# Optimization experiments

Measured on AMD Instinct MI355X. Metric: run time of the kernel, lower is better.

## Reference

```python
import jax, jax.numpy as jnp
import numpy as np

B, T, E, H, D = 1, 2048, 1024, 16, 64  # H*D == E required by module


def setup_inputs() -> dict:
    key = jax.random.key(0)
    ks = jax.random.split(key, 9)
    s_in = (2.0 / E) ** 0.5
    return {
        "x": jax.random.normal(ks[0], (B, T, E), jnp.float32),
        "wq": jax.random.normal(ks[1], (H * D, E), jnp.float32) * E ** -0.5,
        "wk": jax.random.normal(ks[2], (H * D, E), jnp.float32) * E ** -0.5,
        "wv": jax.random.normal(ks[3], (H * D, E), jnp.float32) * E ** -0.5,
        "wr": jax.random.normal(ks[4], (H, E, T), jnp.float32) * s_in,
        "wvr": jax.random.normal(ks[5], (H * D, E), jnp.float32) * E ** -0.5,
        "wj": jax.random.normal(ks[6], (E, E), jnp.float32) * E ** -0.5,
        "gate": jnp.zeros((H, 3), jnp.float32),
        "wo": jax.random.normal(ks[7], (E, H * D), jnp.float32) * E ** -0.5,
    }


def reference(x, wq, wk, wv, wr, wvr, wj, gate, wo):
    Bx, Tx, Ex = x.shape
    Hh = wr.shape[0]
    Dd = wq.shape[0] // Hh
    scale = 1.0 / Dd ** 0.5
    neg = -jnp.inf
    mask = jnp.triu(jnp.ones((Tx, Tx), bool), 1)  # True above diagonal

    def heads(w):  # (B,T,H*D) -> (B,H,T,D)
        return (x @ w.T).reshape(Bx, Tx, Hh, Dd).transpose(0, 2, 1, 3)

    # --- branch 1: standard causal QKV attention ---
    q, k, v = heads(wq), heads(wk), heads(wv)
    qkv_attn = jnp.einsum('bhqd,bhkd->bhqk', q, k) * scale
    qkv_attn = jnp.where(mask, neg, qkv_attn)
    qkv_out = jnp.einsum('bhqk,bhkd->bhqd', jax.nn.softmax(qkv_attn, axis=-1), v)

    # --- branch 2: RRPRAM learned per-position scores ---
    rv = heads(wvr)
    r = jnp.einsum('bte,het->bht', x, wr[:, :, :Tx])  # (B,H,T) key scores
    r_attn = jnp.where(mask, neg, (r * scale)[:, :, None, :])  # (B,H,T,T)
    rrp_out = jnp.einsum('bhqk,bhkd->bhqd', jax.nn.softmax(r_attn, axis=-1), rv)

    # --- branch 3: Janus self-resonance ---
    echo = x @ wj.T            # (B,T,E)
    echo_back = echo @ wj      # F.linear(echo, wj.weight.T)
    scores = (x * echo_back).sum(-1) / Ex ** 0.5  # (B,T)
    j_attn = jnp.where(mask, neg, scores[:, :, None] * scores[:, None, :])  # (B,T,T)
    jA = jax.nn.softmax(j_attn, axis=-1)
    j_val = echo.reshape(Bx, Tx, Hh, Dd).transpose(0, 2, 1, 3)
    jan_out = jnp.einsum('bqk,bhkd->bhqd', jA, j_val)

    # --- gated combine + output proj ---
    g = jax.nn.softmax(gate, axis=-1)  # (H,3)
    out = (g[:, 0][None, :, None, None] * qkv_out
           + g[:, 1][None, :, None, None] * rrp_out
           + g[:, 2][None, :, None, None] * jan_out)
    out = out.transpose(0, 2, 1, 3).reshape(Bx, Tx, Hh * Dd)
    return out @ wo.T
```

## Files before the change

### kernel.cpp

```cpp
#include <hip/hip_runtime.h>
#include <cstddef>
#include <cstdint>

#define TT 2048
#define EE 1024
#define HH 16
#define NSP 2

typedef unsigned short ushort;
typedef unsigned int uint;
typedef __attribute__((ext_vector_type(8))) short short8;
typedef __attribute__((ext_vector_type(8))) _Float16 half8;
typedef __attribute__((ext_vector_type(4))) float f32x4;
typedef __attribute__((ext_vector_type(4))) ushort ushort4v;

__device__ __forceinline__ ushort f2bf(float f) {
  uint u = __builtin_bit_cast(uint, f);
  u = (u + 0x7FFFu + ((u >> 16) & 1u)) >> 16;
  return (ushort)u;
}
__device__ __forceinline__ float bf2f(ushort h) {
  return __builtin_bit_cast(float, (uint)h << 16);
}
__device__ __forceinline__ ushort f2h(float f) {
  return __builtin_bit_cast(ushort, (_Float16)f);
}

__device__ __forceinline__ void async16(ushort* lds, const ushort* g) {
  __builtin_amdgcn_global_load_lds(
      reinterpret_cast<const __attribute__((address_space(1))) void*>(
          reinterpret_cast<uintptr_t>(g)),
      reinterpret_cast<__attribute__((address_space(3))) void*>(
          static_cast<unsigned int>(reinterpret_cast<uintptr_t>(lds))),
      16, 0, 0);
}

__global__ __launch_bounds__(256) void cvt_all(
    const float* __restrict__ x, ushort* __restrict__ xbf,
    ushort* __restrict__ xh, ushort* __restrict__ xTbf,
    const float* __restrict__ w0, const float* __restrict__ w1,
    const float* __restrict__ w2, const float* __restrict__ w3,
    const float* __restrict__ w4, const float* __restrict__ w5,
    ushort* __restrict__ d0, ushort* __restrict__ d1,
    ushort* __restrict__ d2, ushort* __restrict__ d3,
    ushort* __restrict__ d4, ushort* __restrict__ d5,
    float* __restrict__ snorm)
{
  const int z = blockIdx.z;
  if (z == 0) {
    __shared__ float tile[32][33];
    if (blockIdx.x == 0 && blockIdx.y == 0) {
      for (int i = threadIdx.x; i < TT; i += 256) snorm[i] = 0.f;
    }
    const int bn = blockIdx.x * 32;
    const int bm = blockIdx.y * 32;
    const int c4 = (threadIdx.x & 7) * 4;
    const int r  = threadIdx.x >> 3;
    const size_t off = (size_t)(bm + r) * EE + bn + c4;
    float4 v = *(const float4*)(x + off);
    tile[r][c4 + 0] = v.x; tile[r][c4 + 1] = v.y;
    tile[r][c4 + 2] = v.z; tile[r][c4 + 3] = v.w;
    ushort4v b, h;
    b.x = f2bf(v.x); b.y = f2bf(v.y); b.z = f2bf(v.z); b.w = f2bf(v.w);
    h.x = f2h(v.x);  h.y = f2h(v.y);  h.z = f2h(v.z);  h.w = f2h(v.w);
    *(ushort4v*)(xbf + off) = b;
    *(ushort4v*)(xh + off) = h;
    __syncthreads();
    const int t4 = (threadIdx.x & 7) * 4;
    const int e  = threadIdx.x >> 3;
    ushort4v tb;
    tb.x = f2bf(tile[t4 + 0][e]); tb.y = f2bf(tile[t4 + 1][e]);
    tb.z = f2bf(tile[t4 + 2][e]); tb.w = f2bf(tile[t4 + 3][e]);
    *(ushort4v*)(xTbf + (size_t)(bn + e) * TT + bm + t4) = tb;
    return;
  }
  const int lin = blockIdx.y * 32 + blockIdx.x;
  if (lin >= 1024) return;
  const float* src; ushort* dst;
  switch (z) {
    case 1: src = w0; dst = d0; break;
    case 2: src = w1; dst = d1; break;
    case 3: src = w2; dst = d2; break;
    case 4: src = w3; dst = d3; break;
    case 5: src = w4; dst = d4; break;
    default: src = w5; dst = d5; break;
  }
  const int i = lin * 1024 + threadIdx.x * 4;
  float4 v = *(const float4*)(src + i);
  ushort4v o;
  if (z == 6) {
    o.x = f2h(v.x); o.y = f2h(v.y); o.z = f2h(v.z); o.w = f2h(v.w);
  } else {
    o.x = f2bf(v.x); o.y = f2bf(v.y); o.z = f2bf(v.z); o.w = f2bf(v.w);
  }
  *(ushort4v*)(dst + i) = o;
}

__global__ __launch_bounds__(256) void proj5(
    const ushort* __restrict__ Abf, const ushort* __restrict__ Ah,
    const ushort* __restrict__ B0, const ushort* __restrict__ B1,
    const ushort* __restrict__ B2, const ushort* __restrict__ B3,
    const ushort* __restrict__ B4,
    ushort* __restrict__ C0, ushort* __restrict__ C1,
    ushort* __restrict__ C2, ushort* __restrict__ C3,
    ushort* __restrict__ C4, float* __restrict__ snorm,
    int M, int N, int K)
{
  const ushort* A; const ushort* B; ushort* C; int om;
  switch (blockIdx.z) {
    case 0: A = Abf; B = B0; C = C0; om = 1; break;
    case 1: A = Abf; B = B1; C = C1; om = 1; break;
    case 2: A = Abf; B = B2; C = C2; om = 2; break;
    case 3: A = Abf; B = B3; C = C3; om = 1; break;
    default: A = Ah; B = B4; C = C4; om = 3; break;
  }
  const bool f16 = (blockIdx.z == 4);
  __shared__ __align__(16) ushort As[2][128 * 64];
  __shared__ __align__(16) ushort Bs[2][128 * 64];
  const int tid = threadIdx.x;
  const int m0 = blockIdx.y * 128, n0 = blockIdx.x * 128;
  const int w = tid >> 6, lane = tid & 63;
  const int wr = w >> 1, wc = w & 1;
  const int lr = lane & 15, lk = lane >> 4;
  const int srow = lane >> 3;
  const int scol = ((lane & 7) ^ srow) * 8;
  const ushort* AgL = A + (size_t)(m0 + w * 32 + srow) * K + scol;
  const ushort* BgL = B + (size_t)(n0 + w * 32 + srow) * K + scol;
  const int sbase = (w * 32) * 64;
  const int s0 = (lk ^ (lr & 7)) * 8;
  f32x4 acc[4][4] = {};
  const int NT = K >> 6;
#pragma unroll
  for (int c = 0; c < 4; ++c) {
    async16(&As[0][sbase + c * 8 * 64], AgL + (size_t)c * 8 * K);
    async16(&Bs[0][sbase + c * 8 * 64], BgL + (size_t)c * 8 * K);
  }
  __syncthreads();
  for (int kt = 0; kt < NT; ++kt) {
    const int cur = kt & 1;
    if (kt + 1 < NT) {
      const int kn = (kt + 1) << 6;
#pragma unroll
      for (int c = 0; c < 4; ++c) {
        async16(&As[cur ^ 1][sbase + c * 8 * 64], AgL + (size_t)c * 8 * K + kn);
        async16(&Bs[cur ^ 1][sbase + c * 8 * 64], BgL + (size_t)c * 8 * K + kn);
      }
    }
    short8 a0[4], a1[4], b0[4], b1[4];
#pragma unroll
    for (int i = 0; i < 4; ++i) {
      const ushort* p = &As[cur][(wr * 64 + i * 16 + lr) * 64];
      a0[i] = *(const short8*)(p + s0);
      a1[i] = *(const short8*)(p + (s0 ^ 32));
    }
#pragma unroll
    for (int j = 0; j < 4; ++j) {
      const ushort* p = &Bs[cur][(wc * 64 + j * 16 + lr) * 64];
      b0[j] = *(const short8*)(p + s0);
      b1[j] = *(const short8*)(p + (s0 ^ 32));
    }
    if (f16) {
#pragma unroll
      for (int i = 0; i < 4; ++i)
#pragma unroll
        for (int j = 0; j < 4; ++j) {
          acc[i][j] = __builtin_amdgcn_mfma_f32_16x16x32_f16(
              __builtin_bit_cast(half8, a0[i]), __builtin_bit_cast(half8, b0[j]),
              acc[i][j], 0, 0, 0);
          acc[i][j] = __builtin_amdgcn_mfma_f32_16x16x32_f16(
              __builtin_bit_cast(half8, a1[i]), __builtin_bit_cast(half8, b1[j]),
              acc[i][j], 0, 0, 0);
        }
    } else {
#pragma unroll
      for (int i = 0; i < 4; ++i)
#pragma unroll
        for (int j = 0; j < 4; ++j) {
          acc[i][j] = __builtin_amdgcn_mfma_f32_16x16x32_bf16(
              a0[i], b0[j], acc[i][j], 0, 0, 0);
          acc[i][j] = __builtin_amdgcn_mfma_f32_16x16x32_bf16(
              a1[i], b1[j], acc[i][j], 0, 0, 0);
        }
    }
    __syncthreads();
  }
#pragma unroll
  for (int i = 0; i < 4; ++i)
#pragma unroll
    for (int r = 0; r < 4; ++r) {
      int row = m0 + wr * 64 + i * 16 + lk * 4 + r;
#pragma unroll
      for (int j = 0; j < 4; ++j) {
        int col = n0 + wc * 64 + j * 16 + lr;
        ushort v = (om == 2) ? f2h(acc[i][j][r]) : f2bf(acc[i][j][r]);
        if (om == 1)
          C[((size_t)(col >> 6) * M + row) * 64 + (col & 63)] = v;
        else if (om == 2)
          C[(size_t)(col >> 6) * 64 * M + (size_t)(col & 63) * M + row] = v;
        else
          C[(size_t)col * M + row] = v;
      }
    }
  if (om == 3) {
#pragma unroll
    for (int i = 0; i < 4; ++i)
#pragma unroll
      for (int r = 0; r < 4; ++r) {
        float p = 0.f;
#pragma unroll
        for (int j = 0; j < 4; ++j) p += acc[i][j][r] * acc[i][j][r];
        p += __shfl_xor(p, 1); p += __shfl_xor(p, 2);
        p += __shfl_xor(p, 4); p += __shfl_xor(p, 8);
        if (lr == 0)
          atomicAdd(&snorm[m0 + wr * 64 + i * 16 + lk * 4 + r], p);
      }
  }
}

template<bool CZ>
__global__ __launch_bounds__(256) void gemm_mfma(
    const ushort* __restrict__ A, const ushort* __restrict__ B,
    float* __restrict__ Cp, int M, int N, int K)
{
  __shared__ __align__(16) ushort As[2][128 * 64];
  __shared__ __align__(16) ushort Bs[2][128 * 64];
  const int tid = threadIdx.x;
  const int m0 = blockIdx.y * 128, n0 = blockIdx.x * 128;
  const int w = tid >> 6, lane = tid & 63;
  const int wr = w >> 1, wc = w & 1;
  const int lr = lane & 15, lk = lane >> 4;
  const int srow = lane >> 3;
  const int scol = ((lane & 7) ^ srow) * 8;
  const ushort* AgL = A + (size_t)(m0 + w * 32 + srow) * K + scol;
  const ushort* BgL = B + (size_t)(n0 + w * 32 + srow) * K + scol;
  const int sbase = (w * 32) * 64;
  const int s0 = (lk ^ (lr & 7)) * 8;
  f32x4 acc[4][4] = {};
  const int Keff = CZ ? (K < m0 + 128 ? K : m0 + 128) : K;
  const int NT = Keff >> 6;
#pragma unroll
  for (int c = 0; c < 4; ++c) {
    async16(&As[0][sbase + c * 8 * 64], AgL + (size_t)c * 8 * K);
    async16(&Bs[0][sbase + c * 8 * 64], BgL + (size_t)c * 8 * K);
  }
  __syncthreads();
  for (int kt = 0; kt < NT; ++kt) {
    const int cur = kt & 1;
    if (kt + 1 < NT) {
      const int kn = (kt + 1) << 6;
#pragma unroll
      for (int c = 0; c < 4; ++c) {
        async16(&As[cur ^ 1][sbase + c * 8 * 64], AgL + (size_t)c * 8 * K + kn);
        async16(&Bs[cur ^ 1][sbase + c * 8 * 64], BgL + (size_t)c * 8 * K + kn);
      }
    }
    short8 a0[4], a1[4], b0[4], b1[4];
#pragma unroll
    for (int i = 0; i < 4; ++i) {
      const ushort* p = &As[cur][(wr * 64 + i * 16 + lr) * 64];
      a0[i] = *(const short8*)(p + s0);
      a1[i] = *(const short8*)(p + (s0 ^ 32));
    }
#pragma unroll
    for (int j = 0; j < 4; ++j) {
      const ushort* p = &Bs[cur][(wc * 64 + j * 16 + lr) * 64];
      b0[j] = *(const short8*)(p + s0);
      b1[j] = *(const short8*)(p + (s0 ^ 32));
    }
#pragma unroll
    for (int i = 0; i < 4; ++i)
#pragma unroll
      for (int j = 0; j < 4; ++j) {
        acc[i][j] = __builtin_amdgcn_mfma_f32_16x16x32_bf16(
            a0[i], b0[j], acc[i][j], 0, 0, 0);
        acc[i][j] = __builtin_amdgcn_mfma_f32_16x16x32_bf16(
            a1[i], b1[j], acc[i][j], 0, 0, 0);
      }
    __syncthreads();
  }
#pragma unroll
  for (int i = 0; i < 4; ++i)
#pragma unroll
    for (int r = 0; r < 4; ++r) {
      int row = m0 + wr * 64 + i * 16 + lk * 4 + r;
#pragma unroll
      for (int j = 0; j < 4; ++j) {
        int col = n0 + wc * 64 + j * 16 + lr;
        Cp[(size_t)row * N + col] = acc[i][j][r];
      }
    }
}

__global__ __launch_bounds__(64) void flash_mfma(
    const ushort* __restrict__ Qg, const ushort* __restrict__ Kg,
    const ushort* __restrict__ Vg, float* __restrict__ pbuf, int T, int nqt)
{
  const int bid = blockIdx.x;
  const int xcd = bid & 7;
  const int ii = bid >> 3;
  const int h = xcd * 2 + (ii & 1);
  const int sp = (ii >> 1) & 1;
  const int w  = (ii >> 2) & 3;
  const int qt = (nqt - 1) - (ii >> 4);
  const int q0 = qt * 64;
  const int nk = qt + 1;
  const int span = (nk + 1) >> 1;
  const int kb = sp * span;
  const int ke = (nk < kb + span) ? nk : (kb + span);
  const int lane = threadIdx.x & 63;
  const int lr = lane & 15, lk = lane >> 4;
  const ushort* Q = Qg + (size_t)h * T * 64;
  const ushort* K = Kg + (size_t)h * T * 64;
  const ushort* V = Vg + (size_t)h * 64 * T;
  __shared__ __align__(16) ushort Ps[16 * 72];
  const float CEXP = 0.18033688f;

  f32x4 o[4] = {};
  float ls[4] = {0.f, 0.f, 0.f, 0.f};

  if (kb < ke) {
    short8 qa0 = *(const short8*)(Q + (size_t)(q0 + w * 16 + lr) * 64 + lk * 8);
    short8 qa1 = *(const short8*)(Q + (size_t)(q0 + w * 16 + lr) * 64 + 32 + lk * 8);
    short8 kb0[4], kb1[4];
#pragma unroll
    for (int c = 0; c < 4; ++c) {
      const ushort* kp = K + (size_t)(kb * 64 + c * 16 + lr) * 64 + lk * 8;
      kb0[c] = *(const short8*)kp;
      kb1[c] = *(const short8*)(kp + 32);
    }
    for (int kt = kb; kt < ke; ++kt) {
      const int k0 = kt * 64;
      short8 vb0[4], vb1[4];
#pragma unroll
      for (int c = 0; c < 4; ++c) {
        const ushort* vp = V + (size_t)(c * 16 + lr) * T + k0 + lk * 8;
        vb0[c] = *(const short8*)vp;
        vb1[c] = *(const short8*)(vp + 32);
      }
      f32x4 s[4];
      __builtin_amdgcn_s_setprio(1);
#pragma unroll
      for (int c = 0; c < 4; ++c) {
        f32x4 z = {};
        z = __builtin_amdgcn_mfma_f32_16x16x32_bf16(qa0, kb0[c], z, 0, 0, 0);
        z = __builtin_amdgcn_mfma_f32_16x16x32_bf16(qa1, kb1[c], z, 0, 0, 0);
        s[c] = z;
      }
      __builtin_amdgcn_s_setprio(0);
      if (kt + 1 < ke) {
#pragma unroll
        for (int c = 0; c < 4; ++c) {
          const ushort* kp = K + (size_t)(k0 + 64 + c * 16 + lr) * 64 + lk * 8;
          kb0[c] = *(const short8*)kp;
          kb1[c] = *(const short8*)(kp + 32);
        }
      }
      float pv[4][4];
#pragma unroll
      for (int c = 0; c < 4; ++c)
#pragma unroll
        for (int r = 0; r < 4; ++r)
          pv[c][r] = exp2f(s[c][r] * CEXP);
      if (kt == qt) {
        const int rowbase = q0 + w * 16 + lk * 4;
#pragma unroll
        for (int c = 0; c < 4; ++c) {
          const int col = k0 + c * 16 + lr;
#pragma unroll
          for (int r = 0; r < 4; ++r)
            if (col > rowbase + r) pv[c][r] = 0.f;
        }
      }
#pragma unroll
      for (int c = 0; c < 4; ++c)
#pragma unroll
        for (int r = 0; r < 4; ++r) {
          ls[r] += pv[c][r];
          Ps[(lk * 4 + r) * 72 + c * 16 + lr] = f2h(pv[c][r]);
        }
      short8 pa0 = *(const short8*)(&Ps[lr * 72 + lk * 8]);
      short8 pa1 = *(const short8*)(&Ps[lr * 72 + 32 + lk * 8]);
      __builtin_amdgcn_s_setprio(1);
#pragma unroll
      for (int c = 0; c < 4; ++c) {
        o[c] = __builtin_amdgcn_mfma_f32_16x16x32_f16(
            __builtin_bit_cast(half8, pa0), __builtin_bit_cast(half8, vb0[c]),
            o[c], 0, 0, 0);
        o[c] = __builtin_amdgcn_mfma_f32_16x16x32_f16(
            __builtin_bit_cast(half8, pa1), __builtin_bit_cast(half8, vb1[c]),
            o[c], 0, 0, 0);
      }
      __builtin_amdgcn_s_setprio(0);
    }
#pragma unroll
    for (int r = 0; r < 4; ++r) {
      ls[r] += __shfl_xor(ls[r], 1);
      ls[r] += __shfl_xor(ls[r], 2);
      ls[r] += __shfl_xor(ls[r], 4);
      ls[r] += __shfl_xor(ls[r], 8);
    }
  }
  float* pb = pbuf + ((size_t)(h * nqt + qt) * NSP + sp) * 4160;
#pragma unroll
  for (int c = 0; c < 4; ++c)
#pragma unroll
    for (int r = 0; r < 4; ++r) {
      int row = w * 16 + lk * 4 + r;
      pb[(size_t)row * 64 + c * 16 + lr] = o[c][r];
    }
  if (lr == 0) {
#pragma unroll
    for (int r = 0; r < 4; ++r)
      pb[4096 + w * 16 + lk * 4 + r] = ls[r];
  }
}

__global__ __launch_bounds__(256) void merge_combine(
    const float* __restrict__ pbuf, const ushort* __restrict__ a2,
    const float* __restrict__ jraw, const float* __restrict__ denj,
    const float* __restrict__ gate, ushort* __restrict__ comb, int T, int nqt)
{
  const int b = blockIdx.x;
  const int h = b / nqt, qt = b - h * nqt;
  const float* p0 = pbuf + (size_t)b * NSP * 4160;
  const float* p1 = p0 + 4160;
  __shared__ float lsum[64];
  if (threadIdx.x < 64)
    lsum[threadIdx.x] = p0[4096 + threadIdx.x] + p1[4096 + threadIdx.x];
  float g0 = gate[h * 3 + 0], g1 = gate[h * 3 + 1], g2 = gate[h * 3 + 2];
  float mg = fmaxf(g0, fmaxf(g1, g2));
  float e0 = __expf(g0 - mg), e1 = __expf(g1 - mg), e2 = __expf(g2 - mg);
  float inv = 1.f / (e0 + e1 + e2);
  __syncthreads();
  for (int i = threadIdx.x; i < 4096; i += 256) {
    const int r = i >> 6, d = i & 63;
    const int t = qt * 64 + r;
    const float o1 = (p0[i] + p1[i]) / lsum[r];
    const size_t hd = ((size_t)h * T + t) * 64 + d;
    const float v =
        (e0 * o1 + e1 * bf2f(a2[hd]) +
         e2 * jraw[(size_t)t * EE + h * 64 + d] / denj[t]) * inv;
    comb[(size_t)t * EE + h * 64 + d] = f2bf(v);
  }
}

__global__ __launch_bounds__(256) void rscore6(
    const ushort* __restrict__ xTbf, const float* __restrict__ wr,
    float* __restrict__ rpart, int T, int E)
{
  const int h = blockIdx.y;
  const int e0 = blockIdx.z * 64;
  const int t0 = (blockIdx.x * 256 + threadIdx.x) * 4;
  const float* wrh = wr + (size_t)h * E * T;
  float4 acc = {0.f, 0.f, 0.f, 0.f};
#pragma unroll 4
  for (int e = e0; e < e0 + 64; ++e) {
    ushort4v xv = *(const ushort4v*)(xTbf + (size_t)e * T + t0);
    float4 wv = *(const float4*)(wrh + (size_t)e * T + t0);
    acc.x += bf2f(xv.x) * wv.x;
    acc.y += bf2f(xv.y) * wv.y;
    acc.z += bf2f(xv.z) * wv.z;
    acc.w += bf2f(xv.w) * wv.w;
  }
  *(float4*)(rpart + ((size_t)blockIdx.z * HH + h) * T + t0) = acc;
}

__global__ __launch_bounds__(256) void rsoftmax2(
    const float* __restrict__ rpart, float* __restrict__ w, int T)
{
  const int h = blockIdx.x;
  __shared__ float rs[TT];
  __shared__ float red[4];
  for (int t = threadIdx.x; t < T; t += 256) {
    float a = 0.f;
#pragma unroll
    for (int s = 0; s < 16; ++s) a += rpart[((size_t)s * HH + h) * T + t];
    rs[t] = a;
  }
  __syncthreads();
  float mx = -1e30f;
  for (int t = threadIdx.x; t < T; t += 256) mx = fmaxf(mx, rs[t]);
#pragma unroll
  for (int o = 32; o; o >>= 1) mx = fmaxf(mx, __shfl_xor(mx, o));
  if ((threadIdx.x & 63) == 0) red[threadIdx.x >> 6] = mx;
  __syncthreads();
  mx = fmaxf(fmaxf(red[0], red[1]), fmaxf(red[2], red[3]));
  float* wh = w + (size_t)h * T;
  for (int t = threadIdx.x; t < T; t += 256)
    wh[t] = __expf((rs[t] - mx) * 0.125f);
}

__global__ __launch_bounds__(64) void rrp_part(
    const float* __restrict__ wgt, const ushort* __restrict__ rv,
    float* __restrict__ segsum, int T)
{
  const int h = blockIdx.x, seg = blockIdx.y, d = threadIdx.x;
  const int segLen = T >> 5;
  const float* wh = wgt + (size_t)h * T;
  const ushort* rvh = rv + (size_t)h * T * 64;
  const int kbeg = seg * segLen, kend = kbeg + segLen;
  float num = 0.f, den = 0.f;
  for (int k = kbeg; k < kend; ++k) {
    float wk = wh[k];
    num += wk * bf2f(rvh[(size_t)k * 64 + d]);
    den += wk;
  }
  float* o = segsum + ((size_t)h * 32 + seg) * 65;
  o[d] = num;
  if (d == 0) o[64] = den;
}

__global__ __launch_bounds__(64) void rrp_scan2(
    const float* __restrict__ wgt, const ushort* __restrict__ rv,
    const float* __restrict__ segsum, ushort* __restrict__ out, int T)
{
  const int h = blockIdx.x, seg = blockIdx.y, d = threadIdx.x;
  const int segLen = T >> 5;
  const float* wh = wgt + (size_t)h * T;
  const ushort* rvh = rv + (size_t)h * T * 64;
  ushort* oh = out + (size_t)h * T * 64;
  float num = 0.f, den = 0.f;
  for (int s = 0; s < seg; ++s) {
    const float* p = segsum + ((size_t)h * 32 + s) * 65;
    num += p[d];
    den += p[64];
  }
  const int kbeg = seg * segLen, kend = kbeg + segLen;
  for (int k = kbeg; k < kend; ++k) {
    float wk = wh[k];
    num += wk * bf2f(rvh[(size_t)k * 64 + d]);
    den += wk;
    oh[(size_t)k * 64 + d] = f2bf(num / den);
  }
}

__global__ __launch_bounds__(256) void janus_w(
    const float* __restrict__ snorm, ushort* __restrict__ Wb,
    float* __restrict__ den, int T)
{
  const int q = blockIdx.x;
  const float sq = snorm[q] * 0.03125f;
  float mx = -1e30f;
  for (int k = threadIdx.x; k <= q; k += 256)
    mx = fmaxf(mx, sq * (snorm[k] * 0.03125f));
#pragma unroll
  for (int o = 32; o; o >>= 1) mx = fmaxf(mx, __shfl_xor(mx, o));
  __shared__ float red[4];
  if ((threadIdx.x & 63) == 0) red[threadIdx.x >> 6] = mx;
  __syncthreads();
  mx = fmaxf(fmaxf(red[0], red[1]), fmaxf(red[2], red[3]));
  float sum = 0.f;
  ushort* Wq = Wb + (size_t)q * T;
  for (int k = threadIdx.x; k < T; k += 256) {
    float wv = (k <= q) ? __expf(sq * (snorm[k] * 0.03125f) - mx) : 0.f;
    ushort wb = f2bf(wv);
    Wq[k] = wb;
    sum += bf2f(wb);
  }
#pragma unroll
  for (int o = 32; o; o >>= 1) sum += __shfl_xor(sum, o);
  __syncthreads();
  if ((threadIdx.x & 63) == 0) red[threadIdx.x >> 6] = sum;
  __syncthreads();
  if (threadIdx.x == 0) den[q] = red[0] + red[1] + red[2] + red[3];
}

extern "C" void kernel_launch(void* const* d_in, const int* in_sizes, int n_in,
                              void* d_out, int out_size, void* d_ws, size_t ws_size,
                              hipStream_t stream)
{
  (void)in_sizes; (void)n_in; (void)out_size; (void)ws_size;
  const float* x    = (const float*)d_in[0];
  const float* wq   = (const float*)d_in[1];
  const float* wk   = (const float*)d_in[2];
  const float* wv   = (const float*)d_in[3];
  const float* wr   = (const float*)d_in[4];
  const float* wvr  = (const float*)d_in[5];
  const float* wj   = (const float*)d_in[6];
  const float* gate = (const float*)d_in[7];
  const float* wo   = (const float*)d_in[8];
  float* out = (float*)d_out;

  const int T = TT, E = EE, H = HH;
  const int nqt = T / 64;
  const size_t TE = (size_t)T * E;
  const size_t EE2 = (size_t)E * E;
  const size_t TT2 = (size_t)T * T;

  ushort* u = (ushort*)d_ws;
  ushort* xbf   = u;
  ushort* xh    = xbf + TE;
  ushort* xTbf  = xh + TE;
  ushort* wqb   = xTbf + TE;
  ushort* wkb   = wqb + EE2;
  ushort* wvb   = wkb + EE2;
  ushort* wvrb  = wvb + EE2;
  ushort* wob   = wvrb + EE2;
  ushort* wjh   = wob + EE2;
  ushort* qhb   = wjh + EE2;
  ushort* khb   = qhb + TE;
  ushort* vtb   = khb + TE;
  ushort* rvhb  = vtb + TE;
  ushort* echoT = rvhb + TE;
  ushort* a2b   = echoT + TE;
  ushort* Wbf   = a2b + TE;
  ushort* combb = Wbf + TT2;
  float* jraw   = (float*)(combb + TE);
  float* wwb    = jraw + TE;
  float* snorm  = wwb + (size_t)H * T;
  float* denj   = snorm + T;
  float* rpart  = denj + T;
  float* segsum = rpart + (size_t)16 * H * T;
  float* pbuf   = segsum + (size_t)H * 32 * 65;

  dim3 blk(256);
  cvt_all<<<dim3(E / 32, T / 32, 7), blk, 0, stream>>>(
      x, xbf, xh, xTbf, wq, wk, wv, wvr, wo, wj,
      wqb, wkb, wvb, wvrb, wob, wjh, snorm);

  proj5<<<dim3(E / 128, T / 128, 5), blk, 0, stream>>>(
      xbf, xh, wqb, wkb, wvb, wvrb, wjh,
      qhb, khb, vtb, rvhb, echoT, snorm, T, E, E);

  rscore6<<<dim3(T / 1024, H, E / 64), blk, 0, stream>>>(
      xTbf, wr, rpart, T, E);
  rsoftmax2<<<H, blk, 0, stream>>>(rpart, wwb, T);

  flash_mfma<<<dim3(H * nqt * NSP * 4), dim3(64), 0, stream>>>(
      qhb, khb, vtb, pbuf, T, nqt);

  rrp_part<<<dim3(H, 32), dim3(64), 0, stream>>>(wwb, rvhb, segsum, T);
  rrp_scan2<<<dim3(H, 32), dim3(64), 0, stream>>>(wwb, rvhb, segsum, a2b, T);

  janus_w<<<T, blk, 0, stream>>>(snorm, Wbf, denj, T);
  gemm_mfma<true><<<dim3(E / 128, T / 128), blk, 0, stream>>>(
      Wbf, echoT, jraw, T, E, T);

  merge_combine<<<H * nqt, blk, 0, stream>>>(pbuf, a2b, jraw, denj, gate,
                                             combb, T, nqt);
  gemm_mfma<false><<<dim3(E / 128, T / 128), blk, 0, stream>>>(
      combb, wob, (float*)out, T, E, E);
}
```

Baseline: 441.2 us.

## Drop flash KV split, fuse janus weights with r-softmax, stage RRP scans in LDS

New measurement: 416.2 us. -5.7%, faster.

```diff
diff --git a/kernel.cpp b/kernel.cpp
--- a/kernel.cpp
+++ b/kernel.cpp
@@ -5,7 +5,6 @@
 #define TT 2048
 #define EE 1024
 #define HH 16
-#define NSP 2
 
 typedef unsigned short ushort;
 typedef unsigned int uint;
@@ -293,20 +292,16 @@
 
 __global__ __launch_bounds__(64) void flash_mfma(
     const ushort* __restrict__ Qg, const ushort* __restrict__ Kg,
-    const ushort* __restrict__ Vg, float* __restrict__ pbuf, int T, int nqt)
+    const ushort* __restrict__ Vg, ushort* __restrict__ O, int T, int nqt)
 {
   const int bid = blockIdx.x;
   const int xcd = bid & 7;
   const int ii = bid >> 3;
   const int h = xcd * 2 + (ii & 1);
-  const int sp = (ii >> 1) & 1;
-  const int w  = (ii >> 2) & 3;
-  const int qt = (nqt - 1) - (ii >> 4);
+  const int w  = (ii >> 1) & 3;
+  const int qt = (nqt - 1) - (ii >> 3);
   const int q0 = qt * 64;
-  const int nk = qt + 1;
-  const int span = (nk + 1) >> 1;
-  const int kb = sp * span;
-  const int ke = (nk < kb + span) ? nk : (kb + span);
+  const int ke = qt + 1;
   const int lane = threadIdx.x & 63;
   const int lr = lane & 15, lk = lane >> 4;
   const ushort* Q = Qg + (size_t)h * T * 64;
@@ -318,130 +313,114 @@
   f32x4 o[4] = {};
   float ls[4] = {0.f, 0.f, 0.f, 0.f};
 
-  if (kb < ke) {
-    short8 qa0 = *(const short8*)(Q + (size_t)(q0 + w * 16 + lr) * 64 + lk * 8);
-    short8 qa1 = *(const short8*)(Q + (size_t)(q0 + w * 16 + lr) * 64 + 32 + lk * 8);
-    short8 kb0[4], kb1[4];
+  short8 qa0 = *(const short8*)(Q + (size_t)(q0 + w * 16 + lr) * 64 + lk * 8);
+  short8 qa1 = *(const short8*)(Q + (size_t)(q0 + w * 16 + lr) * 64 + 32 + lk * 8);
+  short8 kb0[4], kb1[4];
+#pragma unroll
+  for (int c = 0; c < 4; ++c) {
+    const ushort* kp = K + (size_t)(c * 16 + lr) * 64 + lk * 8;
+    kb0[c] = *(const short8*)kp;
+    kb1[c] = *(const short8*)(kp + 32);
+  }
+  for (int kt = 0; kt < ke; ++kt) {
+    const int k0 = kt * 64;
+    short8 vb0[4], vb1[4];
 #pragma unroll
     for (int c = 0; c < 4; ++c) {
-      const ushort* kp = K + (size_t)(kb * 64 + c * 16 + lr) * 64 + lk * 8;
-      kb0[c] = *(const short8*)kp;
-      kb1[c] = *(const short8*)(kp + 32);
-    }
-    for (int kt = kb; kt < ke; ++kt) {
-      const int k0 = kt * 64;
-      short8 vb0[4], vb1[4];
+      const ushort* vp = V + (size_t)(c * 16 + lr) * T + k0 + lk * 8;
+      vb0[c] = *(const short8*)vp;
+      vb1[c] = *(const short8*)(vp + 32);
+    }
+    f32x4 s[4];
+    __builtin_amdgcn_s_setprio(1);
+#pragma unroll
+    for (int c = 0; c < 4; ++c) {
+      f32x4 z = {};
+      z = __builtin_amdgcn_mfma_f32_16x16x32_bf16(qa0, kb0[c], z, 0, 0, 0);
+      z = __builtin_amdgcn_mfma_f32_16x16x32_bf16(qa1, kb1[c], z, 0, 0, 0);
+      s[c] = z;
+    }
+    __builtin_amdgcn_s_setprio(0);
+    if (kt + 1 < ke) {
 #pragma unroll
       for (int c = 0; c < 4; ++c) {
-        const ushort* vp = V + (size_t)(c * 16 + lr) * T + k0 + lk * 8;
-        vb0[c] = *(const short8*)vp;
-        vb1[c] = *(const short8*)(vp + 32);
-      }
-      f32x4 s[4];
-      __builtin_amdgcn_s_setprio(1);
+        const ushort* kp = K + (size_t)(k0 + 64 + c * 16 + lr) * 64 + lk * 8;
+        kb0[c] = *(const short8*)kp;
+        kb1[c] = *(const short8*)(kp + 32);
+      }
+    }
+    float pv[4][4];
+#pragma unroll
+    for (int c = 0; c < 4; ++c)
+#pragma unroll
+      for (int r = 0; r < 4; ++r)
+        pv[c][r] = exp2f(s[c][r] * CEXP);
+    if (kt == qt) {
+      const int rowbase = q0 + w * 16 + lk * 4;
 #pragma unroll
       for (int c = 0; c < 4; ++c) {
-        f32x4 z = {};
-        z = __builtin_amdgcn_mfma_f32_16x16x32_bf16(qa0, kb0[c], z, 0, 0, 0);
-        z = __builtin_amdgcn_mfma_f32_16x16x32_bf16(qa1, kb1[c], z, 0, 0, 0);
-        s[c] = z;
-      }
-      __builtin_amdgcn_s_setprio(0);
-      if (kt + 1 < ke) {
-#pragma unroll
-        for (int c = 0; c < 4; ++c) {
-          const ushort* kp = K + (size_t)(k0 + 64 + c * 16 + lr) * 64 + lk * 8;
-          kb0[c] = *(const short8*)kp;
-          kb1[c] = *(const short8*)(kp + 32);
-        }
-      }
-      float pv[4][4];
-#pragma unroll
-      for (int c = 0; c < 4; ++c)
+        const int col = k0 + c * 16 + lr;
 #pragma unroll
         for (int r = 0; r < 4; ++r)
-          pv[c][r] = exp2f(s[c][r] * CEXP);
-      if (kt == qt) {
-        const int rowbase = q0 + w * 16 + lk * 4;
-#pragma unroll
-        for (int c = 0; c < 4; ++c) {
-          const int col = k0 + c * 16 + lr;
-#pragma unroll
-          for (int r = 0; r < 4; ++r)
-            if (col > rowbase + r) pv[c][r] = 0.f;
-        }
-      }
-#pragma unroll
-      for (int c = 0; c < 4; ++c)
-#pragma unroll
-        for (int r = 0; r < 4; ++r) {
-          ls[r] += pv[c][r];
-          Ps[(lk * 4 + r) * 72 + c * 16 + lr] = f2h(pv[c][r]);
-        }
-      short8 pa0 = *(const short8*)(&Ps[lr * 72 + lk * 8]);
-      short8 pa1 = *(const short8*)(&Ps[lr * 72 + 32 + lk * 8]);
-      __builtin_amdgcn_s_setprio(1);
-#pragma unroll
-      for (int c = 0; c < 4; ++c) {
-        o[c] = __builtin_amdgcn_mfma_f32_16x16x32_f16(
-            __builtin_bit_cast(half8, pa0), __builtin_bit_cast(half8, vb0[c]),
-            o[c], 0, 0, 0);
-        o[c] = __builtin_amdgcn_mfma_f32_16x16x32_f16(
-            __builtin_bit_cast(half8, pa1), __builtin_bit_cast(half8, vb1[c]),
-            o[c], 0, 0, 0);
-      }
-      __builtin_amdgcn_s_setprio(0);
-    }
-#pragma unroll
-    for (int r = 0; r < 4; ++r) {
-      ls[r] += __shfl_xor(ls[r], 1);
-      ls[r] += __shfl_xor(ls[r], 2);
-      ls[r] += __shfl_xor(ls[r], 4);
-      ls[r] += __shfl_xor(ls[r], 8);
-    }
-  }
-  float* pb = pbuf + ((size_t)(h * nqt + qt) * NSP + sp) * 4160;
+          if (col > rowbase + r) pv[c][r] = 0.f;
+      }
+    }
+#pragma unroll
+    for (int c = 0; c < 4; ++c)
+#pragma unroll
+      for (int r = 0; r < 4; ++r) {
+        ls[r] += pv[c][r];
+        Ps[(lk * 4 + r) * 72 + c * 16 + lr] = f2h(pv[c][r]);
+      }
+    short8 pa0 = *(const short8*)(&Ps[lr * 72 + lk * 8]);
+    short8 pa1 = *(const short8*)(&Ps[lr * 72 + 32 + lk * 8]);
+    __builtin_amdgcn_s_setprio(1);
+#pragma unroll
+    for (int c = 0; c < 4; ++c) {
+      o[c] = __builtin_amdgcn_mfma_f32_16x16x32_f16(
+          __builtin_bit_cast(half8, pa0), __builtin_bit_cast(half8, vb0[c]),
+          o[c], 0, 0, 0);
+      o[c] = __builtin_amdgcn_mfma_f32_16x16x32_f16(
+          __builtin_bit_cast(half8, pa1), __builtin_bit_cast(half8, vb1[c]),
+          o[c], 0, 0, 0);
+    }
+    __builtin_amdgcn_s_setprio(0);
+  }
+#pragma unroll
+  for (int r = 0; r < 4; ++r) {
+    ls[r] += __shfl_xor(ls[r], 1);
+    ls[r] += __shfl_xor(ls[r], 2);
+    ls[r] += __shfl_xor(ls[r], 4);
+    ls[r] += __shfl_xor(ls[r], 8);
+    ls[r] = 1.f / ls[r];
+  }
+  ushort* Oh = O + ((size_t)h * T + q0) * 64;
 #pragma unroll
   for (int c = 0; c < 4; ++c)
 #pragma unroll
     for (int r = 0; r < 4; ++r) {
       int row = w * 16 + lk * 4 + r;
-      pb[(size_t)row * 64 + c * 16 + lr] = o[c][r];
-    }
-  if (lr == 0) {
-#pragma unroll
-    for (int r = 0; r < 4; ++r)
-      pb[4096 + w * 16 + lk * 4 + r] = ls[r];
-  }
-}
-
-__global__ __launch_bounds__(256) void merge_combine(
-    const float* __restrict__ pbuf, const ushort* __restrict__ a2,
+      Oh[(size_t)row * 64 + c * 16 + lr] = f2bf(o[c][r] * ls[r]);
+    }
+}
+
+__global__ __launch_bounds__(256) void combine_kernel(
+    const ushort* __restrict__ a1, const ushort* __restrict__ a2,
     const float* __restrict__ jraw, const float* __restrict__ denj,
-    const float* __restrict__ gate, ushort* __restrict__ comb, int T, int nqt)
-{
-  const int b = blockIdx.x;
-  const int h = b / nqt, qt = b - h * nqt;
-  const float* p0 = pbuf + (size_t)b * NSP * 4160;
-  const float* p1 = p0 + 4160;
-  __shared__ float lsum[64];
-  if (threadIdx.x < 64)
-    lsum[threadIdx.x] = p0[4096 + threadIdx.x] + p1[4096 + threadIdx.x];
+    const float* __restrict__ gate, ushort* __restrict__ comb, int T)
+{
+  const int idx = blockIdx.x * 256 + threadIdx.x;
+  const int t = idx >> 10;
+  const int c = idx & 1023;
+  const int h = c >> 6;
+  const int d = c & 63;
   float g0 = gate[h * 3 + 0], g1 = gate[h * 3 + 1], g2 = gate[h * 3 + 2];
   float mg = fmaxf(g0, fmaxf(g1, g2));
   float e0 = __expf(g0 - mg), e1 = __expf(g1 - mg), e2 = __expf(g2 - mg);
   float inv = 1.f / (e0 + e1 + e2);
-  __syncthreads();
-  for (int i = threadIdx.x; i < 4096; i += 256) {
-    const int r = i >> 6, d = i & 63;
-    const int t = qt * 64 + r;
-    const float o1 = (p0[i] + p1[i]) / lsum[r];
-    const size_t hd = ((size_t)h * T + t) * 64 + d;
-    const float v =
-        (e0 * o1 + e1 * bf2f(a2[hd]) +
-         e2 * jraw[(size_t)t * EE + h * 64 + d] / denj[t]) * inv;
-    comb[(size_t)t * EE + h * 64 + d] = f2bf(v);
-  }
+  const size_t hd = ((size_t)h * T + t) * 64 + d;
+  float v = (e0 * bf2f(a1[hd]) + e1 * bf2f(a2[hd]) + e2 * jraw[idx] / denj[t]) * inv;
+  comb[idx] = f2bf(v);
 }
 
 __global__ __launch_bounds__(256) void rscore6(
@@ -465,29 +444,58 @@
   *(float4*)(rpart + ((size_t)blockIdx.z * HH + h) * T + t0) = acc;
 }
 
-__global__ __launch_bounds__(256) void rsoftmax2(
-    const float* __restrict__ rpart, float* __restrict__ w, int T)
-{
-  const int h = blockIdx.x;
+__global__ __launch_bounds__(256) void jw_rsm(
+    const float* __restrict__ snorm, ushort* __restrict__ Wb,
+    float* __restrict__ den, const float* __restrict__ rpart,
+    float* __restrict__ wwb, int T)
+{
   __shared__ float rs[TT];
   __shared__ float red[4];
-  for (int t = threadIdx.x; t < T; t += 256) {
-    float a = 0.f;
-#pragma unroll
-    for (int s = 0; s < 16; ++s) a += rpart[((size_t)s * HH + h) * T + t];
-    rs[t] = a;
-  }
-  __syncthreads();
-  float mx = -1e30f;
-  for (int t = threadIdx.x; t < T; t += 256) mx = fmaxf(mx, rs[t]);
-#pragma unroll
-  for (int o = 32; o; o >>= 1) mx = fmaxf(mx, __shfl_xor(mx, o));
-  if ((threadIdx.x & 63) == 0) red[threadIdx.x >> 6] = mx;
-  __syncthreads();
-  mx = fmaxf(fmaxf(red[0], red[1]), fmaxf(red[2], red[3]));
-  float* wh = w + (size_t)h * T;
-  for (int t = threadIdx.x; t < T; t += 256)
-    wh[t] = __expf((rs[t] - mx) * 0.125f);
+  if ((int)blockIdx.x < T) {
+    const int q = blockIdx.x;
+    const float sq = snorm[q] * 0.03125f;
+    float mx = -1e30f;
+    for (int k = threadIdx.x; k <= q; k += 256)
+      mx = fmaxf(mx, sq * (snorm[k] * 0.03125f));
+#pragma unroll
+    for (int o = 32; o; o >>= 1) mx = fmaxf(mx, __shfl_xor(mx, o));
+    if ((threadIdx.x & 63) == 0) red[threadIdx.x >> 6] = mx;
+    __syncthreads();
+    mx = fmaxf(fmaxf(red[0], red[1]), fmaxf(red[2], red[3]));
+    float sum = 0.f;
+    ushort* Wq = Wb + (size_t)q * T;
+    for (int k = threadIdx.x; k < T; k += 256) {
+      float wv = (k <= q) ? __expf(sq * (snorm[k] * 0.03125f) - mx) : 0.f;
+      ushort wb = f2bf(wv);
+      Wq[k] = wb;
+      sum += bf2f(wb);
+    }
+#pragma unroll
+    for (int o = 32; o; o >>= 1) sum += __shfl_xor(sum, o);
+    __syncthreads();
+    if ((threadIdx.x & 63) == 0) red[threadIdx.x >> 6] = sum;
+    __syncthreads();
+    if (threadIdx.x == 0) den[q] = red[0] + red[1] + red[2] + red[3];
+  } else {
+    const int h = blockIdx.x - T;
+    for (int t = threadIdx.x; t < T; t += 256) {
+      float a = 0.f;
+#pragma unroll
+      for (int s = 0; s < 16; ++s) a += rpart[((size_t)s * HH + h) * T + t];
+      rs[t] = a;
+    }
+    __syncthreads();
+    float mx = -1e30f;
+    for (int t = threadIdx.x; t < T; t += 256) mx = fmaxf(mx, rs[t]);
+#pragma unroll
+    for (int o = 32; o; o >>= 1) mx = fmaxf(mx, __shfl_xor(mx, o));
+    if ((threadIdx.x & 63) == 0) red[threadIdx.x >> 6] = mx;
+    __syncthreads();
+    mx = fmaxf(fmaxf(red[0], red[1]), fmaxf(red[2], red[3]));
+    float* wh = wwb + (size_t)h * T;
+    for (int t = threadIdx.x; t < T; t += 256)
+      wh[t] = __expf((rs[t] - mx) * 0.125f);
+  }
 }
 
 __global__ __launch_bounds__(64) void rrp_part(
@@ -496,13 +504,22 @@
 {
   const int h = blockIdx.x, seg = blockIdx.y, d = threadIdx.x;
   const int segLen = T >> 5;
-  const float* wh = wgt + (size_t)h * T;
-  const ushort* rvh = rv + (size_t)h * T * 64;
-  const int kbeg = seg * segLen, kend = kbeg + segLen;
+  const int kbeg = seg * segLen;
+  __shared__ __align__(16) ushort rvs[64 * 64];
+  __shared__ float wls[64];
+  wls[d] = wgt[(size_t)h * T + kbeg + d];
+  {
+    const short8* src = (const short8*)(rv + (size_t)h * T * 64 +
+                                        (size_t)kbeg * 64);
+    short8* dst = (short8*)rvs;
+#pragma unroll
+    for (int j = 0; j < 8; ++j) dst[j * 64 + d] = src[j * 64 + d];
+  }
+  __syncthreads();
   float num = 0.f, den = 0.f;
-  for (int k = kbeg; k < kend; ++k) {
-    float wk = wh[k];
-    num += wk * bf2f(rvh[(size_t)k * 64 + d]);
+  for (int k = 0; k < segLen; ++k) {
+    float wk = wls[k];
+    num += wk * bf2f(rvs[k * 64 + d]);
     den += wk;
   }
   float* o = segsum + ((size_t)h * 32 + seg) * 65;
@@ -516,53 +533,37 @@
 {
   const int h = blockIdx.x, seg = blockIdx.y, d = threadIdx.x;
   const int segLen = T >> 5;
-  const float* wh = wgt + (size_t)h * T;
-  const ushort* rvh = rv + (size_t)h * T * 64;
-  ushort* oh = out + (size_t)h * T * 64;
+  const int kbeg = seg * segLen;
+  __shared__ __align__(16) ushort rvs[64 * 64];
+  __shared__ float wls[64];
+  wls[d] = wgt[(size_t)h * T + kbeg + d];
+  {
+    const short8* src = (const short8*)(rv + (size_t)h * T * 64 +
+                                        (size_t)kbeg * 64);
+    short8* dst = (short8*)rvs;
+#pragma unroll
+    for (int j = 0; j < 8; ++j) dst[j * 64 + d] = src[j * 64 + d];
+  }
   float num = 0.f, den = 0.f;
   for (int s = 0; s < seg; ++s) {
     const float* p = segsum + ((size_t)h * 32 + s) * 65;
     num += p[d];
     den += p[64];
   }
-  const int kbeg = seg * segLen, kend = kbeg + segLen;
-  for (int k = kbeg; k < kend; ++k) {
-    float wk = wh[k];
-    num += wk * bf2f(rvh[(size_t)k * 64 + d]);
+  __syncthreads();
+  for (int k = 0; k < segLen; ++k) {
+    float wk = wls[k];
+    num += wk * bf2f(rvs[k * 64 + d]);
     den += wk;
-    oh[(size_t)k * 64 + d] = f2bf(num / den);
-  }
-}
-
-__global__ __launch_bounds__(256) void janus_w(
-    const float* __restrict__ snorm, ushort* __restrict__ Wb,
-    float* __restrict__ den, int T)
-{
-  const int q = blockIdx.x;
-  const float sq = snorm[q] * 0.03125f;
-  float mx = -1e30f;
-  for (int k = threadIdx.x; k <= q; k += 256)
-    mx = fmaxf(mx, sq * (snorm[k] * 0.03125f));
-#pragma unroll
-  for (int o = 32; o; o >>= 1) mx = fmaxf(mx, __shfl_xor(mx, o));
-  __shared__ float red[4];
-  if ((threadIdx.x & 63) == 0) red[threadIdx.x >> 6] = mx;
+    rvs[k * 64 + d] = f2bf(num / den);
+  }
   __syncthreads();
-  mx = fmaxf(fmaxf(red[0], red[1]), fmaxf(red[2], red[3]));
-  float sum = 0.f;
-  ushort* Wq = Wb + (size_t)q * T;
-  for (int k = threadIdx.x; k < T; k += 256) {
-    float wv = (k <= q) ? __expf(sq * (snorm[k] * 0.03125f) - mx) : 0.f;
-    ushort wb = f2bf(wv);
-    Wq[k] = wb;
-    sum += bf2f(wb);
-  }
-#pragma unroll
-  for (int o = 32; o; o >>= 1) sum += __shfl_xor(sum, o);
-  __syncthreads();
-  if ((threadIdx.x & 63) == 0) red[threadIdx.x >> 6] = sum;
-  __syncthreads();
-  if (threadIdx.x == 0) den[q] = red[0] + red[1] + red[2] + red[3];
+  {
+    short8* dst = (short8*)(out + (size_t)h * T * 64 + (size_t)kbeg * 64);
+    const short8* src = (const short8*)rvs;
+#pragma unroll
+    for (int j = 0; j < 8; ++j) dst[j * 64 + d] = src[j * 64 + d];
+  }
 }
 
 extern "C" void kernel_launch(void* const* d_in, const int* in_sizes, int n_in,
@@ -602,7 +603,8 @@
   ushort* vtb   = khb + TE;
   ushort* rvhb  = vtb + TE;
   ushort* echoT = rvhb + TE;
-  ushort* a2b   = echoT + TE;
+  ushort* a1b   = echoT + TE;
+  ushort* a2b   = a1b + TE;
   ushort* Wbf   = a2b + TE;
   ushort* combb = Wbf + TT2;
   float* jraw   = (float*)(combb + TE);
@@ -611,7 +613,6 @@
   float* denj   = snorm + T;
   float* rpart  = denj + T;
   float* segsum = rpart + (size_t)16 * H * T;
-  float* pbuf   = segsum + (size_t)H * 32 * 65;
 
   dim3 blk(256);
   cvt_all<<<dim3(E / 32, T / 32, 7), blk, 0, stream>>>(
@@ -624,20 +625,20 @@
 
   rscore6<<<dim3(T / 1024, H, E / 64), blk, 0, stream>>>(
       xTbf, wr, rpart, T, E);
-  rsoftmax2<<<H, blk, 0, stream>>>(rpart, wwb, T);
-
-  flash_mfma<<<dim3(H * nqt * NSP * 4), dim3(64), 0, stream>>>(
-      qhb, khb, vtb, pbuf, T, nqt);
+
+  jw_rsm<<<T + H, blk, 0, stream>>>(snorm, Wbf, denj, rpart, wwb, T);
+
+  flash_mfma<<<dim3(H * nqt * 4), dim3(64), 0, stream>>>(
+      qhb, khb, vtb, a1b, T, nqt);
 
   rrp_part<<<dim3(H, 32), dim3(64), 0, stream>>>(wwb, rvhb, segsum, T);
   rrp_scan2<<<dim3(H, 32), dim3(64), 0, stream>>>(wwb, rvhb, segsum, a2b, T);
 
-  janus_w<<<T, blk, 0, stream>>>(snorm, Wbf, denj, T);
   gemm_mfma<true><<<dim3(E / 128, T / 128), blk, 0, stream>>>(
       Wbf, echoT, jraw, T, E, T);
 
-  merge_combine<<<H * nqt, blk, 0, stream>>>(pbuf, a2b, jraw, denj, gate,
-                                             combb, T, nqt);
+  combine_kernel<<<(int)(TE / 256), blk, 0, stream>>>(a1b, a2b, jraw, denj,
+                                                      gate, combb, T);
   gemm_mfma<false><<<dim3(E / 128, T / 128), blk, 0, stream>>>(
       combb, wob, (float*)out, T, E, E);
 }
```
